# Performance work log

Hardware: AMD Instinct MI355X
Metric: run time of the kernel (lower is better)

## Reference

```python
import jax, jax.numpy as jnp
import numpy as np

SEQ, D_IN, D_OUT = 4096, 768, 768

def setup_inputs() -> dict:
    key = jax.random.key(0)
    kx, kq, kk, kv = jax.random.split(key, 4)
    s = 1.0 / np.sqrt(D_IN)
    return {
        "x": jax.random.normal(kx, (SEQ, D_IN), dtype=jnp.float32),
        "Wq": jax.random.uniform(kq, (D_IN, D_OUT), jnp.float32, -s, s),
        "Wk": jax.random.uniform(kk, (D_IN, D_OUT), jnp.float32, -s, s),
        "Wv": jax.random.uniform(kv, (D_IN, D_OUT), jnp.float32, -s, s),
    }

def reference(x, Wq, Wk, Wv):
    # x: [S, d_in]; Wq/Wk/Wv: [d_in, d_out] (torch nn.Linear weight transposed)
    q = x @ Wq
    k = x @ Wk
    v = x @ Wv
    scores = (q @ k.T) / jnp.sqrt(jnp.asarray(k.shape[1], q.dtype))  # [S, S]
    weights = jax.nn.softmax(scores, axis=1)
    return weights @ v  # [S, d_out]
```

## Files before the change

### kernel.cpp

```cpp
#include <hip/hip_runtime.h>
#include <hip/hip_bf16.h>

typedef __bf16 bf16x8 __attribute__((ext_vector_type(8)));
typedef float  f32x4  __attribute__((ext_vector_type(4)));
typedef float  f4     __attribute__((ext_vector_type(4)));
typedef unsigned short us4 __attribute__((ext_vector_type(4)));
typedef unsigned short us8 __attribute__((ext_vector_type(8)));

__device__ inline unsigned short f2bf(float f) {
  union { float f; unsigned int u; } v; v.f = f;
  unsigned int r = v.u + 0x7fffu + ((v.u >> 16) & 1u);
  return (unsigned short)(r >> 16);
}
__device__ inline float bf2f(unsigned short u) {
  union { unsigned int u; float f; } v; v.u = (unsigned int)u << 16;
  return v.f;
}

__device__ inline void gload_lds16(const void* g, void* l) {
  __builtin_amdgcn_global_load_lds((const __attribute__((address_space(1))) void*)g,
                                   (__attribute__((address_space(3))) void*)l, 16, 0, 0);
}

__global__ __launch_bounds__(256) void convfused(const float* __restrict__ x,
                                                 const float* __restrict__ Wq,
                                                 const float* __restrict__ Wk,
                                                 const float* __restrict__ Wv,
                                                 unsigned short* __restrict__ xb,
                                                 unsigned short* __restrict__ wt) {
  __shared__ unsigned short tile[32][33];
  if (blockIdx.x < 3072) {
    int i = blockIdx.x * 256 + threadIdx.x;
    f4 v = ((const f4*)x)[i];
    us4 o;
    #pragma unroll
    for (int c = 0; c < 4; ++c) o[c] = f2bf(v[c]);
    ((us4*)xb)[i] = o;
  } else {
    int b = blockIdx.x - 3072;
    int bz = b / 576, rem = b % 576;
    int bx = rem / 24, by = rem % 24;
    const float* W = bz == 0 ? Wq : (bz == 1 ? Wk : Wv);
    int k0 = bx * 32, n0 = by * 32;
    int c = threadIdx.x & 31, r8 = threadIdx.x >> 5;
    #pragma unroll
    for (int p = 0; p < 4; ++p) {
      int r = p * 8 + r8;
      tile[r][c] = f2bf(W[(size_t)(k0 + r) * 768 + n0 + c]);
    }
    __syncthreads();
    #pragma unroll
    for (int p = 0; p < 4; ++p) {
      int r = p * 8 + r8;
      wt[((size_t)bz * 768 + n0 + r) * 768 + k0 + c] = tile[c][r];
    }
  }
}

__global__ __launch_bounds__(256) void transv(const unsigned short* __restrict__ qkv,
                                              unsigned short* __restrict__ vt) {
  __shared__ unsigned short tile[32][33];
  int s0 = blockIdx.x * 32, d0 = blockIdx.y * 32;
  int c = threadIdx.x & 31, r8 = threadIdx.x >> 5;
  #pragma unroll
  for (int p = 0; p < 4; ++p) {
    int r = p * 8 + r8;
    tile[r][c] = qkv[(size_t)(s0 + r) * 2304 + 1536 + d0 + c];
  }
  __syncthreads();
  #pragma unroll
  for (int p = 0; p < 4; ++p) {
    int r = p * 8 + r8;
    vt[(size_t)(d0 + r) * 4096 + s0 + c] = tile[c][r];
  }
}

template <int WAVES, int WM, int WN, int MINW, typename OUT_T, bool DOEXP, bool DOSCALE>
__global__ __launch_bounds__(WAVES * 64, MINW) void gemmdp(const unsigned short* __restrict__ A,
                                                           const unsigned short* __restrict__ B,
                                                           OUT_T* __restrict__ C0,
                                                           OUT_T* __restrict__ C1,
                                                           const float* __restrict__ rowinv,
                                                           int lda, int ldb, int ldc, int kspan,
                                                           int nbx, float cscale) {
  constexpr int BM = WAVES * 32, BN = WAVES * 32;
  constexpr int MF = 2 * WAVES / WM, NF = 2 * WAVES / WN;
  constexpr int SLOT = (BM + BN) * 64;
  __shared__ __align__(16) char lds[4 * SLOT];
  const int tid = threadIdx.x;
  const int w = tid >> 6, l = tid & 63;
  const int wr = w / WN, wc = w % WN;
  const int lr = l & 15, lk = l >> 4;

  const int nwg = gridDim.x;
  const int swz = (blockIdx.x & 7) * (nwg >> 3) + (blockIdx.x >> 3);
  const int bx = swz % nbx, by = swz / nbx;
  const int m0 = by * BM, n0 = bx * BN;
  const int koff0 = blockIdx.y * kspan;
  OUT_T* __restrict__ C = blockIdx.y ? C1 : C0;

  f32x4 acc[MF][NF] = {};

  const int trow = tid >> 2;
  const int koff = ((tid & 3) * 8) ^ (((tid >> 5) & 1) * 16);
  const unsigned short* gA0 = A + (size_t)(m0 + trow) * lda + koff + koff0;
  const unsigned short* gA1 = A + (size_t)(m0 + BM / 2 + trow) * lda + koff + koff0;
  const unsigned short* gB0 = B + (size_t)(n0 + trow) * ldb + koff + koff0;
  const unsigned short* gB1 = B + (size_t)(n0 + BN / 2 + trow) * ldb + koff + koff0;
  const int wave16 = (tid & ~63) * 16;

  auto stage = [&](int slot, int k0) {
    char* base = lds + slot * SLOT;
    gload_lds16(gA0 + k0, base + wave16);
    gload_lds16(gA1 + k0, base + BM * 32 + wave16);
    gload_lds16(gB0 + k0, base + BM * 64 + wave16);
    gload_lds16(gB1 + k0, base + BM * 64 + BN * 32 + wave16);
  };

  const int xorv = ((l >> 3) & 1) << 5;
  const int aoff = (wr * (MF * 16) + lr) * 64 + lk * 16;
  const int boff = BM * 64 + (wc * (NF * 16) + lr) * 64 + lk * 16;

  auto ldfrags = [&](int slot, bf16x8 (&pa)[MF], bf16x8 (&pb)[NF]) {
    const char* sb = lds + slot * SLOT;
    #pragma unroll
    for (int mf = 0; mf < MF; ++mf)
      pa[mf] = *(const bf16x8*)(sb + ((aoff + mf * 1024) ^ xorv));
    #pragma unroll
    for (int nf = 0; nf < NF; ++nf)
      pb[nf] = *(const bf16x8*)(sb + ((boff + nf * 1024) ^ xorv));
  };

  const int nsteps = kspan >> 5;
  bf16x8 fa[MF], fb[NF], ga[MF], gb[NF];

  stage(0, 0); stage(1, 32); stage(2, 64);
  asm volatile("s_waitcnt vmcnt(8)" ::: "memory");
  __builtin_amdgcn_s_barrier();
  ldfrags(0, fa, fb);

  auto step = [&](int s, bf16x8 (&ca)[MF], bf16x8 (&cb)[NF],
                  bf16x8 (&xa)[MF], bf16x8 (&xb2)[NF]) {
    __builtin_amdgcn_sched_barrier(0);
    if (s < nsteps - 2) asm volatile("s_waitcnt vmcnt(4)" ::: "memory");
    else                asm volatile("s_waitcnt vmcnt(0)" ::: "memory");
    __builtin_amdgcn_s_barrier();
    __builtin_amdgcn_sched_barrier(0);

    if (s + 3 < nsteps) stage((s + 3) & 3, (s + 3) << 5);
    if (s + 1 < nsteps) ldfrags((s + 1) & 3, xa, xb2);

    __builtin_amdgcn_s_setprio(1);
    #pragma unroll
    for (int mf = 0; mf < MF; ++mf)
      #pragma unroll
      for (int nf = 0; nf < NF; ++nf)
        acc[mf][nf] = __builtin_amdgcn_mfma_f32_16x16x32_bf16(ca[mf], cb[nf], acc[mf][nf], 0, 0, 0);
    __builtin_amdgcn_s_setprio(0);
  };

  for (int s = 0; s < nsteps; s += 2) {
    step(s,     fa, fb, ga, gb);
    step(s + 1, ga, gb, fa, fb);
  }

  #pragma unroll
  for (int mf = 0; mf < MF; ++mf)
    #pragma unroll
    for (int nf = 0; nf < NF; ++nf)
      #pragma unroll
      for (int i = 0; i < 4; ++i) {
        int r = m0 + wr * (MF * 16) + mf * 16 + lk * 4 + i;
        int c = n0 + wc * (NF * 16) + nf * 16 + lr;
        float v = acc[mf][nf][i] * cscale;
        if constexpr (DOEXP)   v = __expf(v);
        if constexpr (DOSCALE) v *= rowinv[r];
        if constexpr (__is_same(OUT_T, unsigned short)) C[(size_t)r * ldc + c] = f2bf(v);
        else                                            C[(size_t)r * ldc + c] = v;
      }
}

__global__ __launch_bounds__(256) void rowsum(const unsigned short* __restrict__ P,
                                              float* __restrict__ rowinv) {
  const int wv = threadIdx.x >> 6, l = threadIdx.x & 63;
  const int r = blockIdx.x * 4 + wv;
  const unsigned short* row = P + (size_t)r * 4096;
  float sum = 0.f;
  #pragma unroll
  for (int j = 0; j < 8; ++j) {
    us8 v = ((const us8*)row)[l + j * 64];
    #pragma unroll
    for (int c = 0; c < 8; ++c) sum += bf2f(v[c]);
  }
  #pragma unroll
  for (int o = 32; o > 0; o >>= 1) sum += __shfl_xor(sum, o);
  if (l == 0) rowinv[r] = 1.f / sum;
}

__global__ __launch_bounds__(256) void reduce_add(float* __restrict__ out,
                                                  const float* __restrict__ p1) {
  int i = blockIdx.x * 256 + threadIdx.x;
  f4 a = ((const f4*)out)[i];
  f4 b = ((const f4*)p1)[i];
  #pragma unroll
  for (int c = 0; c < 4; ++c) a[c] += b[c];
  ((f4*)out)[i] = a;
}

extern "C" void kernel_launch(void* const* d_in, const int* in_sizes, int n_in,
                              void* d_out, int out_size, void* d_ws, size_t ws_size,
                              hipStream_t stream) {
  const float* x  = (const float*)d_in[0];
  const float* Wq = (const float*)d_in[1];
  const float* Wk = (const float*)d_in[2];
  const float* Wv = (const float*)d_in[3];
  float* out = (float*)d_out;
  char* ws = (char*)d_ws;

  unsigned short* qkv = (unsigned short*)ws;
  unsigned short* P   = (unsigned short*)(ws + 18874368);
  unsigned short* xb  = (unsigned short*)(ws + 18874368);
  unsigned short* wt  = (unsigned short*)(ws + 18874368 + 6291456);
  unsigned short* vt  = (unsigned short*)(ws + 52428800);
  float* rowinvp      = (float*)(ws + 58720256);
  float* p1           = (float*)ws;

  const float qscale = 0.03608439182435161f;

  convfused<<<4800, 256, 0, stream>>>(x, Wq, Wk, Wv, xb, wt);
  gemmdp<4, 2, 2, 2, unsigned short, false, false><<<576, 256, 0, stream>>>(
      xb, wt, qkv, qkv, nullptr, 768, 768, 2304, 768, 18, 1.0f);
  transv<<<dim3(128, 24), 256, 0, stream>>>(qkv, vt);
  gemmdp<8, 2, 4, 2, unsigned short, true, false><<<256, 512, 0, stream>>>(
      qkv, qkv + 768, P, P, nullptr, 2304, 2304, 4096, 768, 16, qscale);
  rowsum<<<1024, 256, 0, stream>>>(P, rowinvp);
  gemmdp<4, 2, 2, 2, float, false, true><<<dim3(192, 2), 256, 0, stream>>>(
      P, vt, out, p1, rowinvp, 4096, 4096, 768, 2048, 6, 1.0f);
  reduce_add<<<3072, 256, 0, stream>>>(out, p1);
}
```

Before: 117.9 us.

## Switch GEMMs to 32x32x16 MFMA and add non-prefetch variant for scores GEMM

Replaces the 16x16x32 bf16 MFMA tiling with 32x32x16 MFMA, with 16-element accumulators per wave sub-block, which changes the LDS fragment indexing and the epilogue row/column mapping. It adds a template flag: the register double-buffered fragment prefetch stays for the projection and PV GEMMs, while the large QK^T GEMM loads fragments just before use to cut register pressure. The larger MFMA shape is meant to reduce LDS fragment reads per flop and raise MFMA throughput. The trade-offs are larger accumulator register use and exposed LDS latency in the non-prefetch path.

```diff
diff --git a/kernel.cpp b/kernel.cpp
--- a/kernel.cpp
+++ b/kernel.cpp
@@ -2,7 +2,7 @@
 #include <hip/hip_bf16.h>
 
 typedef __bf16 bf16x8 __attribute__((ext_vector_type(8)));
-typedef float  f32x4  __attribute__((ext_vector_type(4)));
+typedef float  f32x16 __attribute__((ext_vector_type(16)));
 typedef float  f4     __attribute__((ext_vector_type(4)));
 typedef unsigned short us4 __attribute__((ext_vector_type(4)));
 typedef unsigned short us8 __attribute__((ext_vector_type(8)));
@@ -75,7 +75,7 @@
   }
 }
 
-template <int WAVES, int WM, int WN, int MINW, typename OUT_T, bool DOEXP, bool DOSCALE>
+template <int WAVES, int WM, int WN, int MINW, bool RA, typename OUT_T, bool DOEXP, bool DOSCALE>
 __global__ __launch_bounds__(WAVES * 64, MINW) void gemmdp(const unsigned short* __restrict__ A,
                                                            const unsigned short* __restrict__ B,
                                                            OUT_T* __restrict__ C0,
@@ -84,13 +84,13 @@
                                                            int lda, int ldb, int ldc, int kspan,
                                                            int nbx, float cscale) {
   constexpr int BM = WAVES * 32, BN = WAVES * 32;
-  constexpr int MF = 2 * WAVES / WM, NF = 2 * WAVES / WN;
+  constexpr int MB = WAVES / WM, NB = WAVES / WN;
   constexpr int SLOT = (BM + BN) * 64;
   __shared__ __align__(16) char lds[4 * SLOT];
   const int tid = threadIdx.x;
   const int w = tid >> 6, l = tid & 63;
   const int wr = w / WN, wc = w % WN;
-  const int lr = l & 15, lk = l >> 4;
+  const int l31 = l & 31, lh = l >> 5;
 
   const int nwg = gridDim.x;
   const int swz = (blockIdx.x & 7) * (nwg >> 3) + (blockIdx.x >> 3);
@@ -99,7 +99,7 @@
   const int koff0 = blockIdx.y * kspan;
   OUT_T* __restrict__ C = blockIdx.y ? C1 : C0;
 
-  f32x4 acc[MF][NF] = {};
+  f32x16 acc[MB][NB] = {};
 
   const int trow = tid >> 2;
   const int koff = ((tid & 3) * 8) ^ (((tid >> 5) & 1) * 16);
@@ -118,66 +118,92 @@
   };
 
   const int xorv = ((l >> 3) & 1) << 5;
-  const int aoff = (wr * (MF * 16) + lr) * 64 + lk * 16;
-  const int boff = BM * 64 + (wc * (NF * 16) + lr) * 64 + lk * 16;
-
-  auto ldfrags = [&](int slot, bf16x8 (&pa)[MF], bf16x8 (&pb)[NF]) {
+  const int aoff = (wr * (MB * 32) + l31) * 64 + lh * 16;
+  const int boff = BM * 64 + (wc * (NB * 32) + l31) * 64 + lh * 16;
+
+  auto ldfrags = [&](int slot, bf16x8 (&pa)[MB * 2], bf16x8 (&pb)[NB * 2]) {
     const char* sb = lds + slot * SLOT;
     #pragma unroll
-    for (int mf = 0; mf < MF; ++mf)
-      pa[mf] = *(const bf16x8*)(sb + ((aoff + mf * 1024) ^ xorv));
-    #pragma unroll
-    for (int nf = 0; nf < NF; ++nf)
-      pb[nf] = *(const bf16x8*)(sb + ((boff + nf * 1024) ^ xorv));
+    for (int mb = 0; mb < MB; ++mb)
+      #pragma unroll
+      for (int kk = 0; kk < 2; ++kk)
+        pa[mb * 2 + kk] = *(const bf16x8*)(sb + ((aoff + mb * 2048 + kk * 32) ^ xorv));
+    #pragma unroll
+    for (int nb = 0; nb < NB; ++nb)
+      #pragma unroll
+      for (int kk = 0; kk < 2; ++kk)
+        pb[nb * 2 + kk] = *(const bf16x8*)(sb + ((boff + nb * 2048 + kk * 32) ^ xorv));
   };
 
-  const int nsteps = kspan >> 5;
-  bf16x8 fa[MF], fb[NF], ga[MF], gb[NF];
-
-  stage(0, 0); stage(1, 32); stage(2, 64);
-  asm volatile("s_waitcnt vmcnt(8)" ::: "memory");
-  __builtin_amdgcn_s_barrier();
-  ldfrags(0, fa, fb);
-
-  auto step = [&](int s, bf16x8 (&ca)[MF], bf16x8 (&cb)[NF],
-                  bf16x8 (&xa)[MF], bf16x8 (&xb2)[NF]) {
-    __builtin_amdgcn_sched_barrier(0);
-    if (s < nsteps - 2) asm volatile("s_waitcnt vmcnt(4)" ::: "memory");
-    else                asm volatile("s_waitcnt vmcnt(0)" ::: "memory");
-    __builtin_amdgcn_s_barrier();
-    __builtin_amdgcn_sched_barrier(0);
-
-    if (s + 3 < nsteps) stage((s + 3) & 3, (s + 3) << 5);
-    if (s + 1 < nsteps) ldfrags((s + 1) & 3, xa, xb2);
-
+  auto domfma = [&](bf16x8 (&ca)[MB * 2], bf16x8 (&cb)[NB * 2]) {
     __builtin_amdgcn_s_setprio(1);
     #pragma unroll
-    for (int mf = 0; mf < MF; ++mf)
-      #pragma unroll
-      for (int nf = 0; nf < NF; ++nf)
-        acc[mf][nf] = __builtin_amdgcn_mfma_f32_16x16x32_bf16(ca[mf], cb[nf], acc[mf][nf], 0, 0, 0);
+    for (int kk = 0; kk < 2; ++kk)
+      #pragma unroll
+      for (int mb = 0; mb < MB; ++mb)
+        #pragma unroll
+        for (int nb = 0; nb < NB; ++nb)
+          acc[mb][nb] = __builtin_amdgcn_mfma_f32_32x32x16_bf16(
+              ca[mb * 2 + kk], cb[nb * 2 + kk], acc[mb][nb], 0, 0, 0);
     __builtin_amdgcn_s_setprio(0);
   };
 
-  for (int s = 0; s < nsteps; s += 2) {
-    step(s,     fa, fb, ga, gb);
-    step(s + 1, ga, gb, fa, fb);
-  }
-
-  #pragma unroll
-  for (int mf = 0; mf < MF; ++mf)
-    #pragma unroll
-    for (int nf = 0; nf < NF; ++nf)
-      #pragma unroll
-      for (int i = 0; i < 4; ++i) {
-        int r = m0 + wr * (MF * 16) + mf * 16 + lk * 4 + i;
-        int c = n0 + wc * (NF * 16) + nf * 16 + lr;
-        float v = acc[mf][nf][i] * cscale;
+  const int nsteps = kspan >> 5;
+
+  if constexpr (RA) {
+    bf16x8 fa[MB * 2], fb[NB * 2], ga[MB * 2], gb[NB * 2];
+    stage(0, 0); stage(1, 32); stage(2, 64);
+    asm volatile("s_waitcnt vmcnt(8)" ::: "memory");
+    __builtin_amdgcn_s_barrier();
+    ldfrags(0, fa, fb);
+
+    auto step = [&](int s, bf16x8 (&ca)[MB * 2], bf16x8 (&cb)[NB * 2],
+                    bf16x8 (&xa)[MB * 2], bf16x8 (&xb2)[NB * 2]) {
+      __builtin_amdgcn_sched_barrier(0);
+      if (s < nsteps - 2) asm volatile("s_waitcnt vmcnt(4)" ::: "memory");
+      else                asm volatile("s_waitcnt vmcnt(0)" ::: "memory");
+      __builtin_amdgcn_s_barrier();
+      __builtin_amdgcn_sched_barrier(0);
+      if (s + 3 < nsteps) stage((s + 3) & 3, (s + 3) << 5);
+      if (s + 1 < nsteps) ldfrags((s + 1) & 3, xa, xb2);
+      domfma(ca, cb);
+    };
+    for (int s = 0; s < nsteps; s += 2) {
+      step(s,     fa, fb, ga, gb);
+      step(s + 1, ga, gb, fa, fb);
+    }
+  } else {
+    bf16x8 fa[MB * 2], fb[NB * 2];
+    stage(0, 0); stage(1, 32); stage(2, 64);
+    for (int s = 0; s < nsteps; ++s) {
+      __builtin_amdgcn_sched_barrier(0);
+      if (s < nsteps - 2)       asm volatile("s_waitcnt vmcnt(8)" ::: "memory");
+      else if (s == nsteps - 2) asm volatile("s_waitcnt vmcnt(4)" ::: "memory");
+      else                      asm volatile("s_waitcnt vmcnt(0)" ::: "memory");
+      __builtin_amdgcn_s_barrier();
+      __builtin_amdgcn_sched_barrier(0);
+      if (s + 3 < nsteps) stage((s + 3) & 3, (s + 3) << 5);
+      ldfrags(s & 3, fa, fb);
+      domfma(fa, fb);
+    }
+  }
+
+  #pragma unroll
+  for (int mb = 0; mb < MB; ++mb)
+    #pragma unroll
+    for (int nb = 0; nb < NB; ++nb) {
+      int colg = n0 + wc * (NB * 32) + nb * 32 + l31;
+      int rbase = m0 + wr * (MB * 32) + mb * 32 + 4 * lh;
+      #pragma unroll
+      for (int reg = 0; reg < 16; ++reg) {
+        int r = rbase + (reg & 3) + 8 * (reg >> 2);
+        float v = acc[mb][nb][reg] * cscale;
         if constexpr (DOEXP)   v = __expf(v);
         if constexpr (DOSCALE) v *= rowinv[r];
-        if constexpr (__is_same(OUT_T, unsigned short)) C[(size_t)r * ldc + c] = f2bf(v);
-        else                                            C[(size_t)r * ldc + c] = v;
+        if constexpr (__is_same(OUT_T, unsigned short)) C[(size_t)r * ldc + colg] = f2bf(v);
+        else                                            C[(size_t)r * ldc + colg] = v;
       }
+    }
 }
 
 __global__ __launch_bounds__(256) void rowsum(const unsigned short* __restrict__ P,
@@ -228,13 +254,13 @@
   const float qscale = 0.03608439182435161f;
 
   convfused<<<4800, 256, 0, stream>>>(x, Wq, Wk, Wv, xb, wt);
-  gemmdp<4, 2, 2, 2, unsigned short, false, false><<<576, 256, 0, stream>>>(
+  gemmdp<4, 2, 2, 2, true, unsigned short, false, false><<<576, 256, 0, stream>>>(
       xb, wt, qkv, qkv, nullptr, 768, 768, 2304, 768, 18, 1.0f);
   transv<<<dim3(128, 24), 256, 0, stream>>>(qkv, vt);
-  gemmdp<8, 2, 4, 2, unsigned short, true, false><<<256, 512, 0, stream>>>(
+  gemmdp<8, 2, 4, 2, false, unsigned short, true, false><<<256, 512, 0, stream>>>(
       qkv, qkv + 768, P, P, nullptr, 2304, 2304, 4096, 768, 16, qscale);
   rowsum<<<1024, 256, 0, stream>>>(P, rowinvp);
-  gemmdp<4, 2, 2, 2, float, false, true><<<dim3(192, 2), 256, 0, stream>>>(
+  gemmdp<4, 2, 2, 2, true, float, false, true><<<dim3(192, 2), 256, 0, stream>>>(
       P, vt, out, p1, rowinvp, 4096, 4096, 768, 2048, 6, 1.0f);
   reduce_add<<<3072, 256, 0, stream>>>(out, p1);
 }
```

Measured after the change: 125.1 us. 1.06x slower.

## Compute V transposed directly in projection GEMM and drop transpose kernel

Applied to the files above, without the earlier changes.

The QKV projection GEMM now handles two problems in one launch. The first 384 tiles compute Q and K into a 1536-wide buffer. The remaining 192 tiles compute V^T = Wv^T·x^T straight into the vt layout by swapping the operands. This removes the separate transv kernel launch and its read/write pass over V. The trade-off is a few extra branches and runtime leading dimensions in the GEMM, and a store pattern for V^T with stride 4096.

```diff
diff --git a/kernel.cpp b/kernel.cpp
--- a/kernel.cpp
+++ b/kernel.cpp
@@ -57,32 +57,18 @@
   }
 }
 
-__global__ __launch_bounds__(256) void transv(const unsigned short* __restrict__ qkv,
-                                              unsigned short* __restrict__ vt) {
-  __shared__ unsigned short tile[32][33];
-  int s0 = blockIdx.x * 32, d0 = blockIdx.y * 32;
-  int c = threadIdx.x & 31, r8 = threadIdx.x >> 5;
-  #pragma unroll
-  for (int p = 0; p < 4; ++p) {
-    int r = p * 8 + r8;
-    tile[r][c] = qkv[(size_t)(s0 + r) * 2304 + 1536 + d0 + c];
-  }
-  __syncthreads();
-  #pragma unroll
-  for (int p = 0; p < 4; ++p) {
-    int r = p * 8 + r8;
-    vt[(size_t)(d0 + r) * 4096 + s0 + c] = tile[c][r];
-  }
-}
-
-template <int WAVES, int WM, int WN, int MINW, typename OUT_T, bool DOEXP, bool DOSCALE>
+template <int WAVES, int WM, int WN, int MINW, typename OUT_T, bool DOEXP, bool DOSCALE, bool UNI>
 __global__ __launch_bounds__(WAVES * 64, MINW) void gemmdp(const unsigned short* __restrict__ A,
                                                            const unsigned short* __restrict__ B,
                                                            OUT_T* __restrict__ C0,
                                                            OUT_T* __restrict__ C1,
                                                            const float* __restrict__ rowinv,
-                                                           int lda, int ldb, int ldc, int kspan,
-                                                           int nbx, float cscale) {
+                                                           const unsigned short* __restrict__ A2,
+                                                           const unsigned short* __restrict__ B2,
+                                                           OUT_T* __restrict__ C2,
+                                                           int lda, int ldb, int ldc, int nbx,
+                                                           int lda2, int ldb2, int ldc2, int nbx2,
+                                                           int nsplit, int kspan, float cscale) {
   constexpr int BM = WAVES * 32, BN = WAVES * 32;
   constexpr int MF = 2 * WAVES / WM, NF = 2 * WAVES / WN;
   constexpr int SLOT = (BM + BN) * 64;
@@ -94,19 +80,33 @@
 
   const int nwg = gridDim.x;
   const int swz = (blockIdx.x & 7) * (nwg >> 3) + (blockIdx.x >> 3);
-  const int bx = swz % nbx, by = swz / nbx;
+
+  const unsigned short* Ap = A;
+  const unsigned short* Bp = B;
+  OUT_T* Cp = blockIdx.y ? C1 : C0;
+  int LDA = lda, LDB = ldb, LDC = ldc;
+  int bx, by;
+  if constexpr (UNI) {
+    if (swz < nsplit) { bx = swz % nbx;  by = swz / nbx; }
+    else {
+      int s2 = swz - nsplit;
+      bx = s2 % nbx2; by = s2 / nbx2;
+      Ap = A2; Bp = B2; Cp = C2; LDA = lda2; LDB = ldb2; LDC = ldc2;
+    }
+  } else {
+    bx = swz % nbx; by = swz / nbx;
+  }
   const int m0 = by * BM, n0 = bx * BN;
   const int koff0 = blockIdx.y * kspan;
-  OUT_T* __restrict__ C = blockIdx.y ? C1 : C0;
 
   f32x4 acc[MF][NF] = {};
 
   const int trow = tid >> 2;
   const int koff = ((tid & 3) * 8) ^ (((tid >> 5) & 1) * 16);
-  const unsigned short* gA0 = A + (size_t)(m0 + trow) * lda + koff + koff0;
-  const unsigned short* gA1 = A + (size_t)(m0 + BM / 2 + trow) * lda + koff + koff0;
-  const unsigned short* gB0 = B + (size_t)(n0 + trow) * ldb + koff + koff0;
-  const unsigned short* gB1 = B + (size_t)(n0 + BN / 2 + trow) * ldb + koff + koff0;
+  const unsigned short* gA0 = Ap + (size_t)(m0 + trow) * LDA + koff + koff0;
+  const unsigned short* gA1 = Ap + (size_t)(m0 + BM / 2 + trow) * LDA + koff + koff0;
+  const unsigned short* gB0 = Bp + (size_t)(n0 + trow) * LDB + koff + koff0;
+  const unsigned short* gB1 = Bp + (size_t)(n0 + BN / 2 + trow) * LDB + koff + koff0;
   const int wave16 = (tid & ~63) * 16;
 
   auto stage = [&](int slot, int k0) {
@@ -175,8 +175,8 @@
         float v = acc[mf][nf][i] * cscale;
         if constexpr (DOEXP)   v = __expf(v);
         if constexpr (DOSCALE) v *= rowinv[r];
-        if constexpr (__is_same(OUT_T, unsigned short)) C[(size_t)r * ldc + c] = f2bf(v);
-        else                                            C[(size_t)r * ldc + c] = v;
+        if constexpr (__is_same(OUT_T, unsigned short)) Cp[(size_t)r * LDC + c] = f2bf(v);
+        else                                            Cp[(size_t)r * LDC + c] = v;
       }
 }
 
@@ -228,13 +228,18 @@
   const float qscale = 0.03608439182435161f;
 
   convfused<<<4800, 256, 0, stream>>>(x, Wq, Wk, Wv, xb, wt);
-  gemmdp<4, 2, 2, 2, unsigned short, false, false><<<576, 256, 0, stream>>>(
-      xb, wt, qkv, qkv, nullptr, 768, 768, 2304, 768, 18, 1.0f);
-  transv<<<dim3(128, 24), 256, 0, stream>>>(qkv, vt);
-  gemmdp<8, 2, 4, 2, unsigned short, true, false><<<256, 512, 0, stream>>>(
-      qkv, qkv + 768, P, P, nullptr, 2304, 2304, 4096, 768, 16, qscale);
+  gemmdp<4, 2, 2, 2, unsigned short, false, false, true><<<576, 256, 0, stream>>>(
+      xb, wt, qkv, qkv, nullptr,
+      wt + (size_t)1536 * 768, xb, vt,
+      768, 768, 1536, 12,
+      768, 768, 4096, 32,
+      384, 768, 1.0f);
+  gemmdp<8, 2, 4, 2, unsigned short, true, false, false><<<256, 512, 0, stream>>>(
+      qkv, qkv + 768, P, P, nullptr, nullptr, nullptr, nullptr,
+      1536, 1536, 4096, 16, 0, 0, 0, 0, 0, 768, qscale);
   rowsum<<<1024, 256, 0, stream>>>(P, rowinvp);
-  gemmdp<4, 2, 2, 2, float, false, true><<<dim3(192, 2), 256, 0, stream>>>(
-      P, vt, out, p1, rowinvp, 4096, 4096, 768, 2048, 6, 1.0f);
+  gemmdp<4, 2, 2, 2, float, false, true, false><<<dim3(192, 2), 256, 0, stream>>>(
+      P, vt, out, p1, rowinvp, nullptr, nullptr, nullptr,
+      4096, 4096, 768, 6, 0, 0, 0, 0, 0, 2048, 1.0f);
   reduce_add<<<3072, 256, 0, stream>>>(out, p1);
 }
```

New measurement: 114.8 us (median of 2 runs). 1.03x faster.
